# Kernel optimization log

Measured on AMD Instinct MI355X. Metric: run time of the kernel, lower is better.

The kernel has to match this reference:

```python
import jax, jax.numpy as jnp
import numpy as np

N_ATOMS = 4096
N_EDGES = 131072
NUM_ELEMENTS = 100
NUM_BESSEL = 8
CUTOFF = 6.0
D_NODE = 64
D_MSG = 128
SH_DIM = 9            # l=0,1,2 -> 1+3+5
TP_IN = D_MSG * SH_DIM  # 1152
N_HEADS = 4
HEAD_DIM = D_MSG // N_HEADS


def setup_inputs() -> dict:
    key = jax.random.key(0)
    ks = jax.random.split(key, 20)
    def p(k, shape):
        return jax.random.normal(k, shape, dtype=jnp.float32) * 0.05
    z = lambda n: jnp.zeros((n,), jnp.float32)
    return {
        "atomic_numbers": jax.random.randint(ks[0], (N_ATOMS,), 0, NUM_ELEMENTS),
        "positions": jax.random.normal(ks[1], (N_ATOMS, 3), dtype=jnp.float32),
        "edge_index": jax.random.randint(ks[2], (2, N_EDGES), 0, N_ATOMS),
        "edge_vectors": jax.random.normal(ks[3], (N_EDGES, 3), dtype=jnp.float32),
        "edge_lengths": jax.random.uniform(ks[4], (N_EDGES,), dtype=jnp.float32, minval=0.5, maxval=5.5),
        "embed_table": p(ks[5], (NUM_ELEMENTS, D_NODE)),
        "W_r1": p(ks[6], (NUM_BESSEL, 64)), "b_r1": z(64),
        "W_r2": p(ks[7], (64, D_MSG)), "b_r2": z(D_MSG),
        "W_tp": p(ks[8], (TP_IN, D_MSG)), "b_tp": z(D_MSG),
        "W_m1": p(ks[9], (D_MSG, D_MSG)), "b_m1": z(D_MSG),
        "W_m2": p(ks[10], (D_MSG, D_MSG)), "b_m2": z(D_MSG),
        "W_qkv": p(ks[11], (D_MSG, 3 * D_MSG)), "b_qkv": z(3 * D_MSG),
        "W_ao": p(ks[12], (D_MSG, D_MSG)), "b_ao": z(D_MSG),
        "W_g": p(ks[13], (D_MSG, D_MSG)), "b_g": z(D_MSG),
        "W_o": p(ks[14], (D_MSG, D_MSG)), "b_o": z(D_MSG),
    }


def reference(atomic_numbers, positions, edge_index, edge_vectors, edge_lengths,
              embed_table, W_r1, b_r1, W_r2, b_r2, W_tp, b_tp,
              W_m1, b_m1, W_m2, b_m2, W_qkv, b_qkv, W_ao, b_ao,
              W_g, b_g, W_o, b_o):
    node_features = embed_table[atomic_numbers]  # [N, 64]

    # spherical harmonics (l = 0,1,2 -> 9 features), order as in source
    r = jnp.linalg.norm(edge_vectors, axis=-1, keepdims=True) + 1e-8
    u = edge_vectors / r
    x, y, z = u[:, 0], u[:, 1], u[:, 2]
    sh = jnp.stack([jnp.ones_like(x), y, z, x,
                    3.0 * z * z - 1.0, x * z, y * z, x * y, x * x - y * y], axis=-1)  # [E,9]

    # bessel RBF with cosine cutoff envelope
    freqs = jnp.arange(1, NUM_BESSEL + 1, dtype=jnp.float32) * (np.pi / CUTOFF)
    env = 0.5 * (jnp.cos(edge_lengths * (np.pi / CUTOFF)) + 1.0) * (edge_lengths < CUTOFF).astype(jnp.float32)
    rbf = jnp.sin(edge_lengths[:, None] * freqs) / edge_lengths[:, None] * env[:, None]  # [E,8]

    radial = jax.nn.silu(rbf @ W_r1 + b_r1)
    radial = jax.nn.silu(radial @ W_r2 + b_r2)  # [E,128]

    # per-edge outer product radial x sh, flattened per-l blocks then concatenated
    outer = radial[:, :, None] * sh[:, None, :]  # [E,128,9]
    E = outer.shape[0]
    edge_messages = jnp.concatenate([
        outer[:, :, 0:1].reshape(E, -1),   # l=0 -> 128
        outer[:, :, 1:4].reshape(E, -1),   # l=1 -> 384
        outer[:, :, 4:9].reshape(E, -1),   # l=2 -> 640
    ], axis=-1)                            # [E,1152]
    edge_messages = edge_messages @ W_tp + b_tp  # [E,128]

    # scatter-add aggregation onto destination nodes (index_add_)
    dst = edge_index[1]
    aggregated = jnp.zeros((node_features.shape[0], D_MSG), jnp.float32).at[dst].add(edge_messages)

    combined = jnp.concatenate([node_features, aggregated[:, :D_NODE]], axis=-1)  # [N,128]
    updated = jax.nn.silu(combined @ W_m1 + b_m1) @ W_m2 + b_m2                   # [N,128]

    # multi-head self-attention over all atoms (batch=1, seq=N)
    N = updated.shape[0]
    qkv = updated @ W_qkv + b_qkv
    q, k, v = jnp.split(qkv, 3, axis=-1)
    q = q.reshape(N, N_HEADS, HEAD_DIM)
    k = k.reshape(N, N_HEADS, HEAD_DIM)
    v = v.reshape(N, N_HEADS, HEAD_DIM)
    scores = jnp.einsum('nhd,mhd->hnm', q, k) / np.sqrt(HEAD_DIM).astype(np.float32)
    attn = jax.nn.softmax(scores, axis=-1)
    attended = jnp.einsum('hnm,mhd->nhd', attn, v).reshape(N, D_MSG)
    attended = attended @ W_ao + b_ao

    gate = jax.nn.sigmoid(updated @ W_g + b_g)
    out = gate * attended + (1.0 - gate) * updated
    return out @ W_o + b_o
```

## Files before the change

### kernel.cpp

```cpp
#include <hip/hip_runtime.h>
#include <hip/hip_bf16.h>
#include <math.h>

#define N_ATOMS 4096
#define N_EDGES 131072
#define PI6 0.52359877559829887308f

typedef __attribute__((ext_vector_type(4))) float f32x4;
typedef _Float16 h16;
typedef __attribute__((ext_vector_type(8))) _Float16 half8;

__device__ __forceinline__ float silu_f(float x) { return x / (1.0f + __expf(-x)); }

__device__ __forceinline__ unsigned pk2h(float lo, float hi) {
    h16 a = (h16)lo, b = (h16)hi;
    unsigned short ua, ub;
    __builtin_memcpy(&ua, &a, 2);
    __builtin_memcpy(&ub, &b, 2);
    return ((unsigned)ub << 16) | (unsigned)ua;
}

__global__ void wprep_kernel(const float* __restrict__ Wtp, float* __restrict__ Wsl)
{
    int idx = blockIdx.x * 256 + threadIdx.x;
    int o = idx & 63;
    int c = (idx >> 6) & 127;
    int s = idx >> 13;
    int row = (s == 0) ? c : (s < 4 ? 128 + c * 3 + (s - 1) : 512 + c * 5 + (s - 4));
    Wsl[idx] = Wtp[row * 128 + o];
}

__global__ void count_kernel(const int* __restrict__ eidx, int* __restrict__ deg)
{
    int e = blockIdx.x * 256 + threadIdx.x;
    atomicAdd(&deg[eidx[N_EDGES + e]], 1);
}

__global__ void scan_kernel(const int* __restrict__ deg, int* __restrict__ base,
                            int* __restrict__ cur)
{
    __shared__ int sums[1024];
    const int t = threadIdx.x;
    int v0 = deg[4*t], v1 = deg[4*t+1], v2 = deg[4*t+2], v3 = deg[4*t+3];
    int s = v0 + v1 + v2 + v3;
    sums[t] = s;
    __syncthreads();
    for (int off = 1; off < 1024; off <<= 1) {
        int x = (t >= off) ? sums[t - off] : 0;
        __syncthreads();
        sums[t] += x;
        __syncthreads();
    }
    int excl = (t > 0) ? sums[t - 1] : 0;
    base[4*t]   = excl;             cur[4*t]   = excl;
    base[4*t+1] = excl + v0;        cur[4*t+1] = excl + v0;
    base[4*t+2] = excl + v0 + v1;   cur[4*t+2] = excl + v0 + v1;
    base[4*t+3] = excl + v0 + v1 + v2; cur[4*t+3] = excl + v0 + v1 + v2;
}

__global__ void scatter_kernel(const int* __restrict__ eidx, int* __restrict__ cur,
                               int* __restrict__ sortedE)
{
    int e = blockIdx.x * 256 + threadIdx.x;
    int dst = eidx[N_EDGES + e];
    int p = atomicAdd(&cur[dst], 1);
    sortedE[p] = e;
}

__global__ __launch_bounds__(256) void agg_kernel(
    const float* __restrict__ evec, const float* __restrict__ elen,
    const int* __restrict__ sortedE, const int* __restrict__ base,
    const int* __restrict__ deg, int aoff,
    const float* __restrict__ Wr1, const float* __restrict__ br1,
    const float* __restrict__ Wr2, const float* __restrict__ br2,
    float* __restrict__ Gm)
{
    __shared__ float rbfL[32][9];
    __shared__ float shL[32][9];
    __shared__ __align__(16) float R1L[64][32];
    __shared__ __align__(16) float R2L[32][128];
    __shared__ __align__(16) float Gh[1152];

    const int t = threadIdx.x;
    const int dst = aoff + blockIdx.x;
    const int dg = deg[dst];
    const int bs = base[dst];

    const int ch = t & 127, hh = t >> 7;
    float G[9] = {0.f,0.f,0.f,0.f,0.f,0.f,0.f,0.f,0.f};

    const int nch = (dg + 31) >> 5;
    for (int c = 0; c < nch; ++c) {
        __syncthreads();
        {
            int el = t >> 3, f = t & 7;
            int ce = c * 32 + el;
            float v = 0.f;
            if (ce < dg) {
                int eid = sortedE[bs + ce];
                float len = elen[eid];
                float env = 0.5f * (cosf(len * PI6) + 1.0f) * (len < 6.0f ? 1.0f : 0.0f);
                v = sinf(len * ((float)(f + 1) * PI6)) * (env / len);
            }
            rbfL[el][f] = v;
        }
        if (t < 32) {
            int ce = c * 32 + t;
            float s0=0,s1=0,s2=0,s3=0,s4=0,s5=0,s6=0,s7=0,s8=0;
            if (ce < dg) {
                int eid = sortedE[bs + ce];
                float vx = evec[eid*3], vy = evec[eid*3+1], vz = evec[eid*3+2];
                float r = sqrtf(vx*vx + vy*vy + vz*vz) + 1e-8f;
                float inv = 1.0f / r;
                float x = vx*inv, y = vy*inv, z = vz*inv;
                s0 = 1.0f; s1 = y; s2 = z; s3 = x;
                s4 = 3.0f*z*z - 1.0f; s5 = x*z; s6 = y*z; s7 = x*y; s8 = x*x - y*y;
            }
            shL[t][0]=s0; shL[t][1]=s1; shL[t][2]=s2; shL[t][3]=s3;
            shL[t][4]=s4; shL[t][5]=s5; shL[t][6]=s6; shL[t][7]=s7; shL[t][8]=s8;
        }
        __syncthreads();
        {
            int e = t & 31, kob = (t >> 5) << 3;
            float rb[8];
            #pragma unroll
            for (int f = 0; f < 8; ++f) rb[f] = rbfL[e][f];
            #pragma unroll
            for (int i = 0; i < 8; ++i) {
                int ko = kob + i;
                float acc = br1[ko];
                #pragma unroll
                for (int f = 0; f < 8; ++f)
                    acc = fmaf(rb[f], Wr1[f * 64 + ko], acc);
                R1L[ko][e] = silu_f(acc);
            }
        }
        __syncthreads();
        {
            int e4 = t >> 5, c4 = t & 31;
            f32x4 a0 = {0.f,0.f,0.f,0.f}, a1 = a0, a2 = a0, a3 = a0;
            const float* Wp = Wr2 + c4 * 4;
            #pragma unroll 4
            for (int j = 0; j < 64; ++j) {
                f32x4 r = *(const f32x4*)&R1L[j][e4 * 4];
                f32x4 w = *(const f32x4*)&Wp[j * 128];
                a0 += w * r.x;
                a1 += w * r.y;
                a2 += w * r.z;
                a3 += w * r.w;
            }
            f32x4 b2 = *(const f32x4*)&br2[c4 * 4];
            a0 += b2; a1 += b2; a2 += b2; a3 += b2;
            f32x4 o0, o1, o2, o3;
            #pragma unroll
            for (int q = 0; q < 4; ++q) {
                o0[q] = silu_f(a0[q]); o1[q] = silu_f(a1[q]);
                o2[q] = silu_f(a2[q]); o3[q] = silu_f(a3[q]);
            }
            *(f32x4*)&R2L[e4*4 + 0][c4*4] = o0;
            *(f32x4*)&R2L[e4*4 + 1][c4*4] = o1;
            *(f32x4*)&R2L[e4*4 + 2][c4*4] = o2;
            *(f32x4*)&R2L[e4*4 + 3][c4*4] = o3;
        }
        __syncthreads();
        {
            int rem = dg - c * 32; if (rem > 32) rem = 32;
            int lo = hh * 16;
            int hi = rem < lo + 16 ? rem : lo + 16;
            for (int el = lo; el < hi; ++el) {
                float r2 = R2L[el][ch];
                #pragma unroll
                for (int s = 0; s < 9; ++s) G[s] = fmaf(shL[el][s], r2, G[s]);
            }
        }
    }

    __syncthreads();
    if (hh == 1) {
        #pragma unroll
        for (int s = 0; s < 9; ++s) Gh[s * 128 + ch] = G[s];
    }
    __syncthreads();
    if (hh == 0) {
        #pragma unroll
        for (int s = 0; s < 9; ++s)
            Gm[blockIdx.x * 1152 + s * 128 + ch] = G[s] + Gh[s * 128 + ch];
    }
}

__global__ __launch_bounds__(256) void gemm_gw_part(
    const float* __restrict__ Gm, const float* __restrict__ Wsl,
    float* __restrict__ P)
{
    __shared__ __align__(16) float AT[128][17];
    __shared__ __align__(16) float Ws[128][64];
    const int t  = threadIdx.x;
    const int M0 = blockIdx.x * 16;
    const int kk = blockIdx.y;

    for (int idx = t; idx < 16 * 128; idx += 256) {
        int m = idx >> 7, k = idx & 127;
        AT[k][m] = Gm[(M0 + m) * 1152 + kk * 128 + k];
    }
    for (int idx = t; idx < 128 * 64; idx += 256) {
        int k = idx >> 6, o = idx & 63;
        Ws[k][o] = Wsl[(kk * 128 + k) * 64 + o];
    }
    __syncthreads();

    const int m0 = t & 15;
    const int o0 = (t >> 4) * 4;
    f32x4 acc = {0.f, 0.f, 0.f, 0.f};
    #pragma unroll 4
    for (int k = 0; k < 128; ++k) {
        float a = AT[k][m0];
        f32x4 w = *(const f32x4*)&Ws[k][o0];
        acc += w * a;
    }
    *(f32x4*)&P[((size_t)kk * 2048 + M0 + m0) * 64 + o0] = acc;
}

__global__ void gw_reduce(const float* __restrict__ P, const int* __restrict__ deg,
                          const float* __restrict__ btp, int aoff,
                          float* __restrict__ agg)
{
    int i = blockIdx.x * 256 + threadIdx.x;
    int m = i >> 6, o = i & 63;
    float s = 0.f;
    #pragma unroll
    for (int kk = 0; kk < 9; ++kk) s += P[(size_t)kk * 131072 + i];
    agg[(aoff + m) * 64 + o] = s + (float)deg[aoff + m] * btp[o];
}

__global__ void combined_kernel(const int* __restrict__ an,
                                const float* __restrict__ emb,
                                const float* __restrict__ agg,
                                float* __restrict__ comb)
{
    int i = blockIdx.x * 256 + threadIdx.x;
    if (i < N_ATOMS * 64) {
        int n = i >> 6, d = i & 63;
        comb[n * 128 + d]      = emb[an[n] * 64 + d];
        comb[n * 128 + 64 + d] = agg[n * 64 + d];
    }
}

template <int ACT>
__global__ __launch_bounds__(256, 2) void gemm128(
    const float* __restrict__ A, const float* __restrict__ W,
    const float* __restrict__ bias, float* __restrict__ C, int N,
    const float* __restrict__ aux1, const float* __restrict__ aux2)
{
    __shared__ __align__(16) float AT[128][64];
    __shared__ __align__(16) float Ws[128][64];
    const int t  = threadIdx.x;
    const int M0 = blockIdx.x * 64;
    const int N0 = blockIdx.y * 64;

    for (int idx = t; idx < 64 * 128; idx += 256) {
        int m = idx >> 7, k = idx & 127;
        AT[k][m ^ ((k & 15) << 2)] = A[(M0 + m) * 128 + k];
    }
    for (int idx = t; idx < 128 * 64; idx += 256) {
        int k = idx >> 6, o = idx & 63;
        Ws[k][o] = W[k * N + N0 + o];
    }
    __syncthreads();

    const int m0 = (t & 15) * 4;
    const int o0 = (t >> 4) * 4;
    float acc[4][4] = {};
    #pragma unroll 2
    for (int k = 0; k < 128; ++k) {
        int xs = (k & 15) << 2;
        float4 a4 = *(const float4*)&AT[k][m0 ^ xs];
        float4 w4 = *(const float4*)&Ws[k][o0];
        float av[4] = {a4.x, a4.y, a4.z, a4.w};
        float wv[4] = {w4.x, w4.y, w4.z, w4.w};
        #pragma unroll
        for (int i = 0; i < 4; ++i)
            #pragma unroll
            for (int j = 0; j < 4; ++j)
                acc[i][j] = fmaf(av[i], wv[j], acc[i][j]);
    }

    #pragma unroll
    for (int i = 0; i < 4; ++i) {
        int m = M0 + m0 + i;
        #pragma unroll
        for (int j = 0; j < 4; ++j) {
            int o = N0 + o0 + j;
            float v = acc[i][j] + bias[o];
            if (ACT == 1) v = silu_f(v);
            if (ACT == 2) {
                float sg = 1.0f / (1.0f + __expf(-v));
                v = sg * aux1[m * 128 + o] + (1.0f - sg) * aux2[m * 128 + o];
            }
            C[m * N + o] = v;
        }
    }
}

__global__ void qkvprep_kernel(const float* __restrict__ qkvf,
                               h16* __restrict__ Qh, h16* __restrict__ Kh,
                               h16* __restrict__ VT)
{
    int i = blockIdx.x * 256 + threadIdx.x;
    {
        int d = i & 31, n = (i >> 5) & 4095, h = i >> 17;
        Qh[i] = (h16)(qkvf[n * 384 + h * 32 + d] * 0.17677669529663687f);
        Kh[i] = (h16)(qkvf[n * 384 + 128 + h * 32 + d]);
    }
    {
        int n = i & 4095, dh = i >> 12;
        VT[i] = (h16)qkvf[n * 384 + 256 + dh];
    }
}

__global__ __launch_bounds__(256, 4) void attn_kernel(
    const h16* __restrict__ Qh, const h16* __restrict__ Kh,
    const h16* __restrict__ VT, float* __restrict__ attd)
{
    __shared__ float st[4][64][10];
    const int t = threadIdx.x, w = t >> 6, lane = t & 63;
    const int h = blockIdx.x >> 8, qt = blockIdx.x & 255;
    const int l15 = lane & 15, g = lane >> 4;

    const h16* Kb = Kh + (size_t)h * 4096 * 32;
    const h16* Vb = VT + (size_t)h * 32 * 4096;
    half8 Qf = *(const half8*)(Qh + ((size_t)(h * 4096 + qt * 16 + l15) * 32 + g * 8));

    float m = -1e30f, l = 0.0f;
    f32x4 O0 = {0.f,0.f,0.f,0.f}, O1 = {0.f,0.f,0.f,0.f};
    const f32x4 zf = {0.f,0.f,0.f,0.f};
    const int sAlane = l15 + ((g & 1) << 5);
    const bool hi = g >= 2;

    const int kvbase = w * 1024;
    for (int kt = 0; kt < 32; ++kt) {
        int kv0 = kvbase + kt * 32;
        half8 K0 = *(const half8*)(Kb + ((size_t)(kv0 + l15) * 32 + g * 8));
        half8 K1 = *(const half8*)(Kb + ((size_t)(kv0 + 16 + l15) * 32 + g * 8));
        f32x4 S0 = __builtin_amdgcn_mfma_f32_16x16x32_f16(K0, Qf, zf, 0, 0, 0);
        f32x4 S1 = __builtin_amdgcn_mfma_f32_16x16x32_f16(K1, Qf, zf, 0, 0, 0);

        float tmax = fmaxf(fmaxf(fmaxf(S0.x, S0.y), fmaxf(S0.z, S0.w)),
                           fmaxf(fmaxf(S1.x, S1.y), fmaxf(S1.z, S1.w)));
        tmax = fmaxf(tmax, __shfl_xor(tmax, 16));
        tmax = fmaxf(tmax, __shfl_xor(tmax, 32));
        float mn = fmaxf(m, tmax);
        float c = __expf(m - mn);
        m = mn;
        float p0[4], p1[4];
        float ts = 0.f;
        #pragma unroll
        for (int i = 0; i < 4; ++i) { p0[i] = __expf(S0[i] - mn); ts += p0[i]; }
        #pragma unroll
        for (int i = 0; i < 4; ++i) { p1[i] = __expf(S1[i] - mn); ts += p1[i]; }
        ts += __shfl_xor(ts, 16);
        ts += __shfl_xor(ts, 32);
        l = l * c + ts;
        #pragma unroll
        for (int i = 0; i < 4; ++i) { O0[i] *= c; O1[i] *= c; }

        unsigned A0 = pk2h(p0[0], p0[1]), A1 = pk2h(p0[2], p0[3]);
        unsigned A2 = pk2h(p1[0], p1[1]), A3 = pk2h(p1[2], p1[3]);
        unsigned t0 = (unsigned)__shfl((int)A0, sAlane);
        unsigned t1 = (unsigned)__shfl((int)A1, sAlane);
        unsigned t2 = (unsigned)__shfl((int)A2, sAlane);
        unsigned t3 = (unsigned)__shfl((int)A3, sAlane);
        unsigned u0 = (unsigned)__shfl((int)A0, sAlane + 16);
        unsigned u1 = (unsigned)__shfl((int)A1, sAlane + 16);
        unsigned u2 = (unsigned)__shfl((int)A2, sAlane + 16);
        unsigned u3 = (unsigned)__shfl((int)A3, sAlane + 16);
        union { unsigned u[4]; half8 v; } P;
        P.u[0] = hi ? t2 : t0;
        P.u[1] = hi ? t3 : t1;
        P.u[2] = hi ? u2 : u0;
        P.u[3] = hi ? u3 : u1;

        half8 V0 = *(const half8*)(Vb + ((size_t)l15 * 4096 + kv0 + g * 8));
        half8 V1 = *(const half8*)(Vb + ((size_t)(16 + l15) * 4096 + kv0 + g * 8));
        O0 = __builtin_amdgcn_mfma_f32_16x16x32_f16(V0, P.v, O0, 0, 0, 0);
        O1 = __builtin_amdgcn_mfma_f32_16x16x32_f16(V1, P.v, O1, 0, 0, 0);
    }

    #pragma unroll
    for (int i = 0; i < 4; ++i) { st[w][lane][i] = O0[i]; st[w][lane][4 + i] = O1[i]; }
    st[w][lane][8] = m;
    st[w][lane][9] = l;
    __syncthreads();

    if (w == 0) {
        float M = -1e30f;
        #pragma unroll
        for (int j = 0; j < 4; ++j) M = fmaxf(M, st[j][lane][8]);
        float L = 0.f, o0[4] = {}, o1[4] = {};
        #pragma unroll
        for (int j = 0; j < 4; ++j) {
            float f = __expf(st[j][lane][8] - M);
            L += st[j][lane][9] * f;
            #pragma unroll
            for (int i = 0; i < 4; ++i) {
                o0[i] = fmaf(st[j][lane][i], f, o0[i]);
                o1[i] = fmaf(st[j][lane][4 + i], f, o1[i]);
            }
        }
        float invL = 1.0f / L;
        int nq = qt * 16 + l15;
        #pragma unroll
        for (int i = 0; i < 4; ++i) {
            attd[nq * 128 + h * 32 + g * 4 + i]      = o0[i] * invL;
            attd[nq * 128 + h * 32 + 16 + g * 4 + i] = o1[i] * invL;
        }
    }
}

extern "C" void kernel_launch(void* const* d_in, const int* in_sizes, int n_in,
                              void* d_out, int out_size, void* d_ws, size_t ws_size,
                              hipStream_t stream) {
    const int*   an    = (const int*)d_in[0];
    const int*   eidx  = (const int*)d_in[2];
    const float* evec  = (const float*)d_in[3];
    const float* elen  = (const float*)d_in[4];
    const float* emb   = (const float*)d_in[5];
    const float* Wr1   = (const float*)d_in[6];
    const float* br1   = (const float*)d_in[7];
    const float* Wr2   = (const float*)d_in[8];
    const float* br2   = (const float*)d_in[9];
    const float* Wtp   = (const float*)d_in[10];
    const float* btp   = (const float*)d_in[11];
    const float* Wm1   = (const float*)d_in[12];
    const float* bm1   = (const float*)d_in[13];
    const float* Wm2   = (const float*)d_in[14];
    const float* bm2   = (const float*)d_in[15];
    const float* Wqkv  = (const float*)d_in[16];
    const float* bqkv  = (const float*)d_in[17];
    const float* Wao   = (const float*)d_in[18];
    const float* bao   = (const float*)d_in[19];
    const float* Wg    = (const float*)d_in[20];
    const float* bg    = (const float*)d_in[21];
    const float* Wo    = (const float*)d_in[22];
    const float* bo    = (const float*)d_in[23];

    float* ws    = (float*)d_ws;
    float* agg   = ws;
    float* comb  = agg  + N_ATOMS * 64;
    float* h1    = comb + N_ATOMS * 128;
    float* upd   = h1   + N_ATOMS * 128;
    float* qkvf  = upd  + N_ATOMS * 128;
    float* attd  = qkvf + N_ATOMS * 384;
    float* aob   = attd + N_ATOMS * 128;
    float* Wsl   = aob;
    int*   deg     = (int*)(aob + 73728);
    int*   base    = deg + 4096;
    int*   cur     = base + 4096;
    int*   sortedE = cur + 4096;
    float* Gm    = comb;
    float* Pp    = ws + 2621440;
    float* outp  = comb;
    h16* Qhb = (h16*)comb;
    h16* Khb = Qhb + 4 * 4096 * 32;
    h16* VTb = (h16*)h1;

    hipMemsetAsync(deg, 0, 4096 * sizeof(int), stream);

    count_kernel<<<512, 256, 0, stream>>>(eidx, deg);
    scan_kernel<<<1, 1024, 0, stream>>>(deg, base, cur);
    scatter_kernel<<<512, 256, 0, stream>>>(eidx, cur, sortedE);

    wprep_kernel<<<288, 256, 0, stream>>>(Wtp, Wsl);

    agg_kernel<<<2048, 256, 0, stream>>>(
        evec, elen, sortedE, base, deg, 0, Wr1, br1, Wr2, br2, Gm);
    gemm_gw_part<<<dim3(128, 9), 256, 0, stream>>>(Gm, Wsl, Pp);
    gw_reduce<<<512, 256, 0, stream>>>(Pp, deg, btp, 0, agg);
    agg_kernel<<<2048, 256, 0, stream>>>(
        evec, elen, sortedE, base, deg, 2048, Wr1, br1, Wr2, br2, Gm);
    gemm_gw_part<<<dim3(128, 9), 256, 0, stream>>>(Gm, Wsl, Pp);
    gw_reduce<<<512, 256, 0, stream>>>(Pp, deg, btp, 2048, agg);

    combined_kernel<<<(N_ATOMS * 64) / 256, 256, 0, stream>>>(an, emb, agg, comb);

    gemm128<1><<<dim3(64, 2), 256, 0, stream>>>(comb, Wm1, bm1, h1, 128, nullptr, nullptr);
    gemm128<0><<<dim3(64, 2), 256, 0, stream>>>(h1, Wm2, bm2, upd, 128, nullptr, nullptr);
    gemm128<0><<<dim3(64, 6), 256, 0, stream>>>(upd, Wqkv, bqkv, qkvf, 384, nullptr, nullptr);

    qkvprep_kernel<<<2048, 256, 0, stream>>>(qkvf, Qhb, Khb, VTb);

    attn_kernel<<<1024, 256, 0, stream>>>(Qhb, Khb, VTb, attd);

    gemm128<0><<<dim3(64, 2), 256, 0, stream>>>(attd, Wao, bao, aob, 128, nullptr, nullptr);
    gemm128<2><<<dim3(64, 2), 256, 0, stream>>>(upd, Wg, bg, outp, 128, aob, upd);
    gemm128<0><<<dim3(64, 2), 256, 0, stream>>>(outp, Wo, bo, (float*)d_out, 128, nullptr, nullptr);
}
```

Baseline: 315.7 us.

## Restructure edge aggregation per-wavefront and fuse prep kernels into GEMMs

```diff
diff --git a/kernel.cpp b/kernel.cpp
--- a/kernel.cpp
+++ b/kernel.cpp
@@ -18,16 +18,6 @@
     __builtin_memcpy(&ua, &a, 2);
     __builtin_memcpy(&ub, &b, 2);
     return ((unsigned)ub << 16) | (unsigned)ua;
-}
-
-__global__ void wprep_kernel(const float* __restrict__ Wtp, float* __restrict__ Wsl)
-{
-    int idx = blockIdx.x * 256 + threadIdx.x;
-    int o = idx & 63;
-    int c = (idx >> 6) & 127;
-    int s = idx >> 13;
-    int row = (s == 0) ? c : (s < 4 ? 128 + c * 3 + (s - 1) : 512 + c * 5 + (s - 4));
-    Wsl[idx] = Wtp[row * 128 + o];
 }
 
 __global__ void count_kernel(const int* __restrict__ eidx, int* __restrict__ deg)
@@ -75,121 +65,104 @@
     const float* __restrict__ Wr2, const float* __restrict__ br2,
     float* __restrict__ Gm)
 {
-    __shared__ float rbfL[32][9];
-    __shared__ float shL[32][9];
-    __shared__ __align__(16) float R1L[64][32];
-    __shared__ __align__(16) float R2L[32][128];
-    __shared__ __align__(16) float Gh[1152];
-
     const int t = threadIdx.x;
-    const int dst = aoff + blockIdx.x;
+    const int lane = t & 63;
+    const int wv = t >> 6;
+    const int aloc = blockIdx.x * 4 + wv;
+    const int dst = aoff + aloc;
     const int dg = deg[dst];
     const int bs = base[dst];
-
-    const int ch = t & 127, hh = t >> 7;
-    float G[9] = {0.f,0.f,0.f,0.f,0.f,0.f,0.f,0.f,0.f};
-
-    const int nch = (dg + 31) >> 5;
-    for (int c = 0; c < nch; ++c) {
-        __syncthreads();
-        {
-            int el = t >> 3, f = t & 7;
-            int ce = c * 32 + el;
-            float v = 0.f;
+    const int c2 = lane * 2;
+
+    float wr1[8];
+    #pragma unroll
+    for (int f = 0; f < 8; ++f) wr1[f] = Wr1[f * 64 + lane];
+    const float br1v = br1[lane];
+    const float2 b2v = *(const float2*)&br2[c2];
+
+    float G[9][2] = {};
+
+    for (int c0 = 0; c0 < dg; c0 += 2) {
+        float rbf[2][8], sh[2][9];
+        #pragma unroll
+        for (int e = 0; e < 2; ++e) {
+            int ce = c0 + e;
             if (ce < dg) {
                 int eid = sortedE[bs + ce];
                 float len = elen[eid];
-                float env = 0.5f * (cosf(len * PI6) + 1.0f) * (len < 6.0f ? 1.0f : 0.0f);
-                v = sinf(len * ((float)(f + 1) * PI6)) * (env / len);
-            }
-            rbfL[el][f] = v;
-        }
-        if (t < 32) {
-            int ce = c * 32 + t;
-            float s0=0,s1=0,s2=0,s3=0,s4=0,s5=0,s6=0,s7=0,s8=0;
-            if (ce < dg) {
-                int eid = sortedE[bs + ce];
+                float th  = len * PI6;
+                float snt = sinf(th), cst = cosf(th);
+                float env = 0.5f * (cst + 1.0f) * (len < 6.0f ? 1.0f : 0.0f);
+                float invl = env / len;
+                float cc2 = 2.0f * cst;
+                float skm = 0.f, sk = snt;
+                #pragma unroll
+                for (int f = 0; f < 8; ++f) {
+                    rbf[e][f] = sk * invl;
+                    float nx = fmaf(cc2, sk, -skm);
+                    skm = sk; sk = nx;
+                }
                 float vx = evec[eid*3], vy = evec[eid*3+1], vz = evec[eid*3+2];
                 float r = sqrtf(vx*vx + vy*vy + vz*vz) + 1e-8f;
                 float inv = 1.0f / r;
                 float x = vx*inv, y = vy*inv, z = vz*inv;
-                s0 = 1.0f; s1 = y; s2 = z; s3 = x;
-                s4 = 3.0f*z*z - 1.0f; s5 = x*z; s6 = y*z; s7 = x*y; s8 = x*x - y*y;
-            }
-            shL[t][0]=s0; shL[t][1]=s1; shL[t][2]=s2; shL[t][3]=s3;
-            shL[t][4]=s4; shL[t][5]=s5; shL[t][6]=s6; shL[t][7]=s7; shL[t][8]=s8;
-        }
-        __syncthreads();
+                sh[e][0] = 1.0f; sh[e][1] = y; sh[e][2] = z; sh[e][3] = x;
+                sh[e][4] = 3.0f*z*z - 1.0f; sh[e][5] = x*z; sh[e][6] = y*z;
+                sh[e][7] = x*y; sh[e][8] = x*x - y*y;
+            } else {
+                #pragma unroll
+                for (int f = 0; f < 8; ++f) rbf[e][f] = 0.f;
+                #pragma unroll
+                for (int s = 0; s < 9; ++s) sh[e][s] = 0.f;
+            }
+        }
+        float r1_0, r1_1;
         {
-            int e = t & 31, kob = (t >> 5) << 3;
-            float rb[8];
-            #pragma unroll
-            for (int f = 0; f < 8; ++f) rb[f] = rbfL[e][f];
-            #pragma unroll
-            for (int i = 0; i < 8; ++i) {
-                int ko = kob + i;
-                float acc = br1[ko];
-                #pragma unroll
-                for (int f = 0; f < 8; ++f)
-                    acc = fmaf(rb[f], Wr1[f * 64 + ko], acc);
-                R1L[ko][e] = silu_f(acc);
-            }
-        }
-        __syncthreads();
+            float a0 = br1v, a1 = br1v;
+            #pragma unroll
+            for (int f = 0; f < 8; ++f) {
+                a0 = fmaf(rbf[0][f], wr1[f], a0);
+                a1 = fmaf(rbf[1][f], wr1[f], a1);
+            }
+            r1_0 = silu_f(a0);
+            r1_1 = silu_f(a1);
+        }
+        float a00 = 0.f, a01 = 0.f, a10 = 0.f, a11 = 0.f;
+        #pragma unroll 8
+        for (int j = 0; j < 64; ++j) {
+            float2 w = *(const float2*)&Wr2[j * 128 + c2];
+            float s0 = __shfl(r1_0, j);
+            float s1 = __shfl(r1_1, j);
+            a00 = fmaf(s0, w.x, a00);
+            a01 = fmaf(s0, w.y, a01);
+            a10 = fmaf(s1, w.x, a10);
+            a11 = fmaf(s1, w.y, a11);
+        }
         {
-            int e4 = t >> 5, c4 = t & 31;
-            f32x4 a0 = {0.f,0.f,0.f,0.f}, a1 = a0, a2 = a0, a3 = a0;
-            const float* Wp = Wr2 + c4 * 4;
-            #pragma unroll 4
-            for (int j = 0; j < 64; ++j) {
-                f32x4 r = *(const f32x4*)&R1L[j][e4 * 4];
-                f32x4 w = *(const f32x4*)&Wp[j * 128];
-                a0 += w * r.x;
-                a1 += w * r.y;
-                a2 += w * r.z;
-                a3 += w * r.w;
-            }
-            f32x4 b2 = *(const f32x4*)&br2[c4 * 4];
-            a0 += b2; a1 += b2; a2 += b2; a3 += b2;
-            f32x4 o0, o1, o2, o3;
-            #pragma unroll
-            for (int q = 0; q < 4; ++q) {
-                o0[q] = silu_f(a0[q]); o1[q] = silu_f(a1[q]);
-                o2[q] = silu_f(a2[q]); o3[q] = silu_f(a3[q]);
-            }
-            *(f32x4*)&R2L[e4*4 + 0][c4*4] = o0;
-            *(f32x4*)&R2L[e4*4 + 1][c4*4] = o1;
-            *(f32x4*)&R2L[e4*4 + 2][c4*4] = o2;
-            *(f32x4*)&R2L[e4*4 + 3][c4*4] = o3;
-        }
-        __syncthreads();
-        {
-            int rem = dg - c * 32; if (rem > 32) rem = 32;
-            int lo = hh * 16;
-            int hi = rem < lo + 16 ? rem : lo + 16;
-            for (int el = lo; el < hi; ++el) {
-                float r2 = R2L[el][ch];
-                #pragma unroll
-                for (int s = 0; s < 9; ++s) G[s] = fmaf(shL[el][s], r2, G[s]);
-            }
-        }
-    }
-
-    __syncthreads();
-    if (hh == 1) {
-        #pragma unroll
-        for (int s = 0; s < 9; ++s) Gh[s * 128 + ch] = G[s];
-    }
-    __syncthreads();
-    if (hh == 0) {
-        #pragma unroll
-        for (int s = 0; s < 9; ++s)
-            Gm[blockIdx.x * 1152 + s * 128 + ch] = G[s] + Gh[s * 128 + ch];
+            float ra = silu_f(a00 + b2v.x), rb = silu_f(a01 + b2v.y);
+            #pragma unroll
+            for (int s = 0; s < 9; ++s) {
+                G[s][0] = fmaf(sh[0][s], ra, G[s][0]);
+                G[s][1] = fmaf(sh[0][s], rb, G[s][1]);
+            }
+            float rc = silu_f(a10 + b2v.x), rd = silu_f(a11 + b2v.y);
+            #pragma unroll
+            for (int s = 0; s < 9; ++s) {
+                G[s][0] = fmaf(sh[1][s], rc, G[s][0]);
+                G[s][1] = fmaf(sh[1][s], rd, G[s][1]);
+            }
+        }
+    }
+
+    #pragma unroll
+    for (int s = 0; s < 9; ++s) {
+        float2 g2 = make_float2(G[s][0], G[s][1]);
+        *(float2*)&Gm[(size_t)aloc * 1152 + s * 128 + c2] = g2;
     }
 }
 
 __global__ __launch_bounds__(256) void gemm_gw_part(
-    const float* __restrict__ Gm, const float* __restrict__ Wsl,
+    const float* __restrict__ Gm, const float* __restrict__ Wtp,
     float* __restrict__ P)
 {
     __shared__ __align__(16) float AT[128][17];
@@ -204,7 +177,9 @@
     }
     for (int idx = t; idx < 128 * 64; idx += 256) {
         int k = idx >> 6, o = idx & 63;
-        Ws[k][o] = Wsl[(kk * 128 + k) * 64 + o];
+        int row = (kk == 0) ? k : (kk < 4 ? 128 + k * 3 + (kk - 1)
+                                          : 512 + k * 5 + (kk - 4));
+        Ws[k][o] = Wtp[row * 128 + o];
     }
     __syncthreads();
 
@@ -232,24 +207,10 @@
     agg[(aoff + m) * 64 + o] = s + (float)deg[aoff + m] * btp[o];
 }
 
-__global__ void combined_kernel(const int* __restrict__ an,
-                                const float* __restrict__ emb,
-                                const float* __restrict__ agg,
-                                float* __restrict__ comb)
-{
-    int i = blockIdx.x * 256 + threadIdx.x;
-    if (i < N_ATOMS * 64) {
-        int n = i >> 6, d = i & 63;
-        comb[n * 128 + d]      = emb[an[n] * 64 + d];
-        comb[n * 128 + 64 + d] = agg[n * 64 + d];
-    }
-}
-
-template <int ACT>
-__global__ __launch_bounds__(256, 2) void gemm128(
-    const float* __restrict__ A, const float* __restrict__ W,
-    const float* __restrict__ bias, float* __restrict__ C, int N,
-    const float* __restrict__ aux1, const float* __restrict__ aux2)
+__global__ __launch_bounds__(256, 2) void gemm_m1(
+    const int* __restrict__ an, const float* __restrict__ emb,
+    const float* __restrict__ agg, const float* __restrict__ W,
+    const float* __restrict__ bias, float* __restrict__ C)
 {
     __shared__ __align__(16) float AT[128][64];
     __shared__ __align__(16) float Ws[128][64];
@@ -259,11 +220,13 @@
 
     for (int idx = t; idx < 64 * 128; idx += 256) {
         int m = idx >> 7, k = idx & 127;
-        AT[k][m ^ ((k & 15) << 2)] = A[(M0 + m) * 128 + k];
+        float v = (k < 64) ? emb[an[M0 + m] * 64 + k]
+                           : agg[(M0 + m) * 64 + (k - 64)];
+        AT[k][m ^ ((k & 15) << 2)] = v;
     }
     for (int idx = t; idx < 128 * 64; idx += 256) {
         int k = idx >> 6, o = idx & 63;
-        Ws[k][o] = W[k * N + N0 + o];
+        Ws[k][o] = W[k * 128 + N0 + o];
     }
     __syncthreads();
 
@@ -290,8 +253,57 @@
         #pragma unroll
         for (int j = 0; j < 4; ++j) {
             int o = N0 + o0 + j;
+            C[m * 128 + o] = silu_f(acc[i][j] + bias[o]);
+        }
+    }
+}
+
+template <int ACT>
+__global__ __launch_bounds__(256, 2) void gemm128(
+    const float* __restrict__ A, const float* __restrict__ W,
+    const float* __restrict__ bias, float* __restrict__ C, int N,
+    const float* __restrict__ aux1, const float* __restrict__ aux2)
+{
+    __shared__ __align__(16) float AT[128][64];
+    __shared__ __align__(16) float Ws[128][64];
+    const int t  = threadIdx.x;
+    const int M0 = blockIdx.x * 64;
+    const int N0 = blockIdx.y * 64;
+
+    for (int idx = t; idx < 64 * 128; idx += 256) {
+        int m = idx >> 7, k = idx & 127;
+        AT[k][m ^ ((k & 15) << 2)] = A[(M0 + m) * 128 + k];
+    }
+    for (int idx = t; idx < 128 * 64; idx += 256) {
+        int k = idx >> 6, o = idx & 63;
+        Ws[k][o] = W[k * N + N0 + o];
+    }
+    __syncthreads();
+
+    const int m0 = (t & 15) * 4;
+    const int o0 = (t >> 4) * 4;
+    float acc[4][4] = {};
+    #pragma unroll 2
+    for (int k = 0; k < 128; ++k) {
+        int xs = (k & 15) << 2;
+        float4 a4 = *(const float4*)&AT[k][m0 ^ xs];
+        float4 w4 = *(const float4*)&Ws[k][o0];
+        float av[4] = {a4.x, a4.y, a4.z, a4.w};
+        float wv[4] = {w4.x, w4.y, w4.z, w4.w};
+        #pragma unroll
+        for (int i = 0; i < 4; ++i)
+            #pragma unroll
+            for (int j = 0; j < 4; ++j)
+                acc[i][j] = fmaf(av[i], wv[j], acc[i][j]);
+    }
+
+    #pragma unroll
+    for (int i = 0; i < 4; ++i) {
+        int m = M0 + m0 + i;
+        #pragma unroll
+        for (int j = 0; j < 4; ++j) {
+            int o = N0 + o0 + j;
             float v = acc[i][j] + bias[o];
-            if (ACT == 1) v = silu_f(v);
             if (ACT == 2) {
                 float sg = 1.0f / (1.0f + __expf(-v));
                 v = sg * aux1[m * 128 + o] + (1.0f - sg) * aux2[m * 128 + o];
@@ -301,19 +313,61 @@
     }
 }
 
-__global__ void qkvprep_kernel(const float* __restrict__ qkvf,
-                               h16* __restrict__ Qh, h16* __restrict__ Kh,
-                               h16* __restrict__ VT)
-{
-    int i = blockIdx.x * 256 + threadIdx.x;
-    {
-        int d = i & 31, n = (i >> 5) & 4095, h = i >> 17;
-        Qh[i] = (h16)(qkvf[n * 384 + h * 32 + d] * 0.17677669529663687f);
-        Kh[i] = (h16)(qkvf[n * 384 + 128 + h * 32 + d]);
-    }
-    {
-        int n = i & 4095, dh = i >> 12;
-        VT[i] = (h16)qkvf[n * 384 + 256 + dh];
+__global__ __launch_bounds__(256, 2) void gemm_qkv(
+    const float* __restrict__ A, const float* __restrict__ W,
+    const float* __restrict__ bias,
+    h16* __restrict__ Qh, h16* __restrict__ Kh, h16* __restrict__ VT)
+{
+    __shared__ __align__(16) float AT[128][64];
+    __shared__ __align__(16) float Ws[128][64];
+    const int t  = threadIdx.x;
+    const int M0 = blockIdx.x * 64;
+    const int N0 = blockIdx.y * 64;
+
+    for (int idx = t; idx < 64 * 128; idx += 256) {
+        int m = idx >> 7, k = idx & 127;
+        AT[k][m ^ ((k & 15) << 2)] = A[(M0 + m) * 128 + k];
+    }
+    for (int idx = t; idx < 128 * 64; idx += 256) {
+        int k = idx >> 6, o = idx & 63;
+        Ws[k][o] = W[k * 384 + N0 + o];
+    }
+    __syncthreads();
+
+    const int m0 = (t & 15) * 4;
+    const int o0 = (t >> 4) * 4;
+    float acc[4][4] = {};
+    #pragma unroll 2
+    for (int k = 0; k < 128; ++k) {
+        int xs = (k & 15) << 2;
+        float4 a4 = *(const float4*)&AT[k][m0 ^ xs];
+        float4 w4 = *(const float4*)&Ws[k][o0];
+        float av[4] = {a4.x, a4.y, a4.z, a4.w};
+        float wv[4] = {w4.x, w4.y, w4.z, w4.w};
+        #pragma unroll
+        for (int i = 0; i < 4; ++i)
+            #pragma unroll
+            for (int j = 0; j < 4; ++j)
+                acc[i][j] = fmaf(av[i], wv[j], acc[i][j]);
+    }
+
+    const float scale = 0.17677669529663687f;
+    #pragma unroll
+    for (int i = 0; i < 4; ++i) {
+        int m = M0 + m0 + i;
+        #pragma unroll
+        for (int j = 0; j < 4; ++j) {
+            int o = N0 + o0 + j;
+            float v = acc[i][j] + bias[o];
+            if (o < 128) {
+                Qh[((size_t)(o >> 5) * 4096 + m) * 32 + (o & 31)] = (h16)(v * scale);
+            } else if (o < 256) {
+                int oo = o - 128;
+                Kh[((size_t)(oo >> 5) * 4096 + m) * 32 + (oo & 31)] = (h16)v;
+            } else {
+                VT[(size_t)(o - 256) * 4096 + m] = (h16)v;
+            }
+        }
     }
 }
 
@@ -448,11 +502,9 @@
     float* comb  = agg  + N_ATOMS * 64;
     float* h1    = comb + N_ATOMS * 128;
     float* upd   = h1   + N_ATOMS * 128;
-    float* qkvf  = upd  + N_ATOMS * 128;
-    float* attd  = qkvf + N_ATOMS * 384;
-    float* aob   = attd + N_ATOMS * 128;
-    float* Wsl   = aob;
-    int*   deg     = (int*)(aob + 73728);
+    float* attd  = ws + 3407872;
+    float* aob   = ws + 3932160;
+    int*   deg     = (int*)aob;
     int*   base    = deg + 4096;
     int*   cur     = base + 4096;
     int*   sortedE = cur + 4096;
@@ -469,24 +521,18 @@
     scan_kernel<<<1, 1024, 0, stream>>>(deg, base, cur);
     scatter_kernel<<<512, 256, 0, stream>>>(eidx, cur, sortedE);
 
-    wprep_kernel<<<288, 256, 0, stream>>>(Wtp, Wsl);
-
-    agg_kernel<<<2048, 256, 0, stream>>>(
+    agg_kernel<<<512, 256, 0, stream>>>(
         evec, elen, sortedE, base, deg, 0, Wr1, br1, Wr2, br2, Gm);
-    gemm_gw_part<<<dim3(128, 9), 256, 0, stream>>>(Gm, Wsl, Pp);
+    gemm_gw_part<<<dim3(128, 9), 256, 0, stream>>>(Gm, Wtp, Pp);
     gw_reduce<<<512, 256, 0, stream>>>(Pp, deg, btp, 0, agg);
-    agg_kernel<<<2048, 256, 0, stream>>>(
+    agg_kernel<<<512, 256, 0, stream>>>(
         evec, elen, sortedE, base, deg, 2048, Wr1, br1, Wr2, br2, Gm);
-    gemm_gw_part<<<dim3(128, 9), 256, 0, stream>>>(Gm, Wsl, Pp);
+    gemm_gw_part<<<dim3(128, 9), 256, 0, stream>>>(Gm, Wtp, Pp);
     gw_reduce<<<512, 256, 0, stream>>>(Pp, deg, btp, 2048, agg);
 
-    combined_kernel<<<(N_ATOMS * 64) / 256, 256, 0, stream>>>(an, emb, agg, comb);
-
-    gemm128<1><<<dim3(64, 2), 256, 0, stream>>>(comb, Wm1, bm1, h1, 128, nullptr, nullptr);
+    gemm_m1<<<dim3(64, 2), 256, 0, stream>>>(an, emb, agg, Wm1, bm1, h1);
     gemm128<0><<<dim3(64, 2), 256, 0, stream>>>(h1, Wm2, bm2, upd, 128, nullptr, nullptr);
-    gemm128<0><<<dim3(64, 6), 256, 0, stream>>>(upd, Wqkv, bqkv, qkvf, 384, nullptr, nullptr);
-
-    qkvprep_kernel<<<2048, 256, 0, stream>>>(qkvf, Qhb, Khb, VTb);
+    gemm_qkv<<<dim3(64, 6), 256, 0, stream>>>(upd, Wqkv, bqkv, Qhb, Khb, VTb);
 
     attn_kernel<<<1024, 256, 0, stream>>>(Qhb, Khb, VTb, attd);
 
```

New measurement: 417.0 us. 1.32x slower.
